# Performance work log

Measured on AMD Instinct MI355X. Metric: run time of the kernel, lower is better.

The kernel has to match this reference:

```python
import jax, jax.numpy as jnp
import numpy as np

B, T, F, H, OUT, L = 4096, 336, 12, 50, 1, 3


def _lstm_layer(x_tbf, W_ih, W_hh, b_ih, b_hh):
    """PyTorch-semantics LSTM layer. x_tbf: [T,B,in]; returns [T,B,H]."""
    Hh = W_hh.shape[1]
    Bsz = x_tbf.shape[1]
    # precompute input projection for all timesteps: [T,B,4H]
    xz = jnp.einsum('tbf,gf->tbg', x_tbf, W_ih) + (b_ih + b_hh)

    def step(carry, xz_t):
        h, c = carry
        z = xz_t + h @ W_hh.T  # [B,4H]
        i, f, g, o = jnp.split(z, 4, axis=-1)  # PyTorch gate order i,f,g,o
        c = jax.nn.sigmoid(f) * c + jax.nn.sigmoid(i) * jnp.tanh(g)
        h = jax.nn.sigmoid(o) * jnp.tanh(c)
        return (h, c), h

    h0 = jnp.zeros((Bsz, Hh), x_tbf.dtype)
    c0 = jnp.zeros((Bsz, Hh), x_tbf.dtype)
    _, hs = jax.lax.scan(step, (h0, c0), xz)
    return hs


def setup_inputs() -> dict:
    key = jax.random.key(0)
    ks = jax.random.split(key, 16)
    s = 1.0 / np.sqrt(H)  # PyTorch LSTM init scale
    inp = {"x": jax.random.normal(ks[0], (B, T, F), dtype=jnp.float32)}
    in_sizes = [F, H, H]
    k = 1
    for l in range(L):
        inp[f"W_ih_{l}"] = jax.random.uniform(ks[k], (4 * H, in_sizes[l]), jnp.float32, -s, s); k += 1
        inp[f"W_hh_{l}"] = jax.random.uniform(ks[k], (4 * H, H), jnp.float32, -s, s); k += 1
        inp[f"b_ih_{l}"] = jax.random.uniform(ks[k], (4 * H,), jnp.float32, -s, s); k += 1
        inp[f"b_hh_{l}"] = jax.random.uniform(ks[k], (4 * H,), jnp.float32, -s, s); k += 1
    inp["W_lin"] = jax.random.uniform(ks[13], (OUT, H), jnp.float32, -s, s)
    inp["b_lin"] = jax.random.uniform(ks[14], (OUT,), jnp.float32, -s, s)
    return inp


def reference(x, W_ih_0, W_hh_0, b_ih_0, b_hh_0,
              W_ih_1, W_hh_1, b_ih_1, b_hh_1,
              W_ih_2, W_hh_2, b_ih_2, b_hh_2,
              W_lin, b_lin):
    h = jnp.transpose(x, (1, 0, 2))  # [T,B,F] time-major for scan
    params = [(W_ih_0, W_hh_0, b_ih_0, b_hh_0),
              (W_ih_1, W_hh_1, b_ih_1, b_hh_1),
              (W_ih_2, W_hh_2, b_ih_2, b_hh_2)]
    for W_ih, W_hh, bi, bh in params:
        h = _lstm_layer(h, W_ih, W_hh, bi, bh)  # [T,B,H]
    last = h[-1]  # out[:, -1, :] in batch_first layout
    return last @ W_lin.T + b_lin  # [B,OUT]
```

## Files before the change

### kernel.cpp

```cpp
#include <hip/hip_runtime.h>


#define Bsz 4096
#define Tt  336
#define BT  16
#define NTH 1024
#define NTILE 13

typedef _Float16 half8 __attribute__((ext_vector_type(8)));
typedef float    floatx4 __attribute__((ext_vector_type(4)));

struct __align__(16) SMem {
  _Float16 act0[2][BT * 64];
  _Float16 act1[2][BT * 128];
  _Float16 act2[2][BT * 128];
};

__device__ __forceinline__ int offA0(int n, int L) {
  return n * 64 + ((((L >> 3) ^ n) & 7) << 3) + (L & 7);
}
__device__ __forceinline__ int offA12(int n, int L) {
  return n * 128 + ((((L >> 3) ^ n) & 15) << 3) + (L & 7);
}

__device__ __forceinline__ float lstm_cell(floatx4 z, float& c) {
  float ei = __builtin_amdgcn_exp2f(z[0]);
  float ef = __builtin_amdgcn_exp2f(z[1]);
  float eg = __builtin_amdgcn_exp2f(z[2]);
  float eo = __builtin_amdgcn_exp2f(z[3]);
  float ig = __builtin_amdgcn_rcpf(1.f + ei);
  float fg = __builtin_amdgcn_rcpf(1.f + ef);
  float rg = __builtin_amdgcn_rcpf(1.f + eg);
  float og = __builtin_amdgcn_rcpf(1.f + eo);
  float gg = 1.f - 2.f * rg;
  c = fg * c + ig * gg;
  float ec = __builtin_amdgcn_exp2f(2.885390082f * c);
  float rc = __builtin_amdgcn_rcpf(1.f + ec);
  return og * (1.f - 2.f * rc);
}

__device__ __forceinline__ half8 wfrag(const float* __restrict__ Wih,
                                       const float* __restrict__ Whh,
                                       int lenih, int bound, int R, int k0) {
  half8 r = {};
  int u = R >> 2, g = R & 3;
  float sc = (g == 2) ? 2.885390082f : -1.442695041f;
  if (u < 50) {
    int row = g * 50 + u;
#pragma unroll
    for (int j = 0; j < 8; ++j) {
      int k = k0 + j;
      float v = 0.f;
      if (k < bound)           v = Wih[row * lenih + k];
      else if (k < bound + 50) v = Whh[row * 50 + (k - bound)];
      r[j] = (_Float16)(sc * v);
    }
  }
  return r;
}

#define MFMA(a, b, acc) __builtin_amdgcn_mfma_f32_16x16x32_f16((a), (b), (acc), 0, 0, 0)

__global__ __launch_bounds__(NTH, 4)
void lstm_mfma_kernel(const float* __restrict__ x,
                      const float* __restrict__ Wih0, const float* __restrict__ Whh0,
                      const float* __restrict__ bih0, const float* __restrict__ bhh0,
                      const float* __restrict__ Wih1, const float* __restrict__ Whh1,
                      const float* __restrict__ bih1, const float* __restrict__ bhh1,
                      const float* __restrict__ Wih2, const float* __restrict__ Whh2,
                      const float* __restrict__ bih2, const float* __restrict__ bhh2,
                      const float* __restrict__ Wlin, const float* __restrict__ blin,
                      float* __restrict__ out) {
  __shared__ SMem sm;
  const int tid  = threadIdx.x;
  const int blk  = blockIdx.x;
  const int lane = tid & 63;
  const int w    = tid >> 6;
  const int n    = lane & 15;
  const int q    = lane >> 4;
  const bool hasTile = (w < NTILE);
  const int u    = 4 * w + q;
  const bool uok = hasTile && (u < 50);
  const int uc   = (u < 50) ? u : 0;

  {
    int* zp = (int*)&sm;
    for (int i = tid; i < (int)(sizeof(SMem) / 4); i += NTH) zp[i] = 0;
  }

  half8 a0f[2] = {}, a1f[4] = {}, a2f[4] = {};
  floatx4 bia0 = {0,0,0,0}, bia1 = {0,0,0,0}, bia2 = {0,0,0,0};
  if (hasTile) {
    int R = 16 * w + n;
#pragma unroll
    for (int kc = 0; kc < 2; ++kc)
      a0f[kc] = wfrag(Wih0, Whh0, 12, 12, R, kc * 32 + q * 8);
#pragma unroll
    for (int kc = 0; kc < 4; ++kc) {
      a1f[kc] = wfrag(Wih1, Whh1, 50, 50, R, kc * 32 + q * 8);
      a2f[kc] = wfrag(Wih2, Whh2, 50, 50, R, kc * 32 + q * 8);
    }
    if (u < 50) {
#pragma unroll
      for (int g = 0; g < 4; ++g) {
        float sc = (g == 2) ? 2.885390082f : -1.442695041f;
        bia0[g] = sc * (bih0[g * 50 + u] + bhh0[g * 50 + u]);
        bia1[g] = sc * (bih1[g * 50 + u] + bhh1[g * 50 + u]);
        bia2[g] = sc * (bih2[g * 50 + u] + bhh2[g * 50 + u]);
      }
    }
  }

  const int ro0[2] = { offA0(n, q * 8), offA0(n, 32 + q * 8) };
  const int ro1[4] = { offA12(n, q * 8),      offA12(n, 32 + q * 8),
                       offA12(n, 64 + q * 8), offA12(n, 96 + q * 8) };
  const int wr0 = offA0 (n, 12 + uc);
  const int wrA = offA12(n, uc);
  const int wrB = offA12(n, 50 + uc);

  const int tid0 = tid - NTILE * 64;
  const int sr = (tid0 >= 0) ? tid0 / 12 : 0;
  const int sf = (tid0 >= 0) ? tid0 - sr * 12 : 0;
  const int sxo = offA0(sr, sf);
  const float* xp = x + ((size_t)(blk * BT + sr) * Tt) * 12 + sf;
  float xnext = 0.f;

  __syncthreads();
  if (!hasTile) {
    sm.act0[0][sxo] = (_Float16)xp[0];
    xnext = xp[12];
  }
  __syncthreads();

  float c0 = 0.f, c1 = 0.f, c2 = 0.f;

#define STEP(p, t)                                                         \
  {                                                                        \
    if (hasTile) {                                                         \
      half8 b0 = *(const half8*)&sm.act0[p][ro0[0]];                       \
      half8 b1 = *(const half8*)&sm.act0[p][ro0[1]];                       \
      floatx4 z = bia0;                                                    \
      z = MFMA(a0f[0], b0, z);                                             \
      z = MFMA(a0f[1], b1, z);                                             \
      float h = lstm_cell(z, c0);                                          \
      _Float16 hh = (_Float16)h;                                           \
      if (uok) { sm.act0[1 - (p)][wr0] = hh; sm.act1[p][wrA] = hh; }       \
    } else {                                                               \
      if ((t) + 1 < Tt) sm.act0[1 - (p)][sxo] = (_Float16)xnext;           \
      xnext = ((t) + 2 < Tt) ? xp[((t) + 2) * 12] : 0.f;                   \
    }                                                                      \
    __syncthreads();                                                       \
    if (hasTile) {                                                         \
      half8 b0 = *(const half8*)&sm.act1[p][ro1[0]];                       \
      half8 b1 = *(const half8*)&sm.act1[p][ro1[1]];                       \
      half8 b2 = *(const half8*)&sm.act1[p][ro1[2]];                       \
      half8 b3 = *(const half8*)&sm.act1[p][ro1[3]];                       \
      floatx4 z = bia1;                                                    \
      z = MFMA(a1f[0], b0, z);                                             \
      z = MFMA(a1f[1], b1, z);                                             \
      z = MFMA(a1f[2], b2, z);                                             \
      z = MFMA(a1f[3], b3, z);                                             \
      float h = lstm_cell(z, c1);                                          \
      _Float16 hh = (_Float16)h;                                           \
      if (uok) { sm.act1[1 - (p)][wrB] = hh; sm.act2[p][wrA] = hh; }       \
    }                                                                      \
    __syncthreads();                                                       \
    if (hasTile) {                                                         \
      half8 b0 = *(const half8*)&sm.act2[p][ro1[0]];                       \
      half8 b1 = *(const half8*)&sm.act2[p][ro1[1]];                       \
      half8 b2 = *(const half8*)&sm.act2[p][ro1[2]];                       \
      half8 b3 = *(const half8*)&sm.act2[p][ro1[3]];                       \
      floatx4 z = bia2;                                                    \
      z = MFMA(a2f[0], b0, z);                                             \
      z = MFMA(a2f[1], b1, z);                                             \
      z = MFMA(a2f[2], b2, z);                                             \
      z = MFMA(a2f[3], b3, z);                                             \
      float h = lstm_cell(z, c2);                                          \
      if (uok) sm.act2[1 - (p)][wrB] = (_Float16)h;                        \
    }                                                                      \
     \
     \
     \
  }

  for (int t = 0; t < Tt; t += 2) {
    STEP(0, t)
    STEP(1, t + 1)
  }
#undef STEP

  __syncthreads();

  if (tid < BT) {
    float s = blin[0];
    for (int uu = 0; uu < 50; ++uu)
      s += Wlin[uu] * (float)sm.act2[0][offA12(tid, 50 + uu)];
    out[blk * BT + tid] = s;
  }
}

extern "C" void kernel_launch(void* const* d_in, const int* in_sizes, int n_in,
                              void* d_out, int out_size, void* d_ws, size_t ws_size,
                              hipStream_t stream) {
  const float* x    = (const float*)d_in[0];
  const float* Wih0 = (const float*)d_in[1];
  const float* Whh0 = (const float*)d_in[2];
  const float* bih0 = (const float*)d_in[3];
  const float* bhh0 = (const float*)d_in[4];
  const float* Wih1 = (const float*)d_in[5];
  const float* Whh1 = (const float*)d_in[6];
  const float* bih1 = (const float*)d_in[7];
  const float* bhh1 = (const float*)d_in[8];
  const float* Wih2 = (const float*)d_in[9];
  const float* Whh2 = (const float*)d_in[10];
  const float* bih2 = (const float*)d_in[11];
  const float* bhh2 = (const float*)d_in[12];
  const float* Wlin = (const float*)d_in[13];
  const float* blin = (const float*)d_in[14];
  float* outp = (float*)d_out;

  dim3 grid(Bsz / BT);
  dim3 block(NTH);
  lstm_mfma_kernel<<<grid, block, 0, stream>>>(
      x, Wih0, Whh0, bih0, bhh0, Wih1, Whh1, bih1, bhh1,
      Wih2, Whh2, bih2, bhh2, Wlin, blin, outp);
}
```

Baseline: 477.0 us.

## Wavefront-pipeline the three LSTM layers across timesteps with one barrier per tick

Replaces the per-timestep sequence of three layer stages separated by three barriers with a diagonal wavefront schedule. At each tick, layer 0 runs step t, layer 1 runs step t-1 and layer 2 runs step t-2. All three read their inputs from the previous tick's buffers, so only one __syncthreads is needed per tick and the MFMA chains of the three layers can overlap. A prologue and an epilogue fill and drain the pipeline, adding two extra ticks. Buffer parity for the inter-layer handoff changes to write the 1-p slot, which must line up exactly with the skewed indices.

```diff
diff --git a/kernel.cpp b/kernel.cpp
--- a/kernel.cpp
+++ b/kernel.cpp
@@ -134,62 +134,72 @@
 
   float c0 = 0.f, c1 = 0.f, c2 = 0.f;
 
-#define STEP(p, t)                                                         \
+#define TICK(p, DO0, DO1, DO2, t0)                                         \
   {                                                                        \
     if (hasTile) {                                                         \
-      half8 b0 = *(const half8*)&sm.act0[p][ro0[0]];                       \
-      half8 b1 = *(const half8*)&sm.act0[p][ro0[1]];                       \
-      floatx4 z = bia0;                                                    \
-      z = MFMA(a0f[0], b0, z);                                             \
-      z = MFMA(a0f[1], b1, z);                                             \
-      float h = lstm_cell(z, c0);                                          \
-      _Float16 hh = (_Float16)h;                                           \
-      if (uok) { sm.act0[1 - (p)][wr0] = hh; sm.act1[p][wrA] = hh; }       \
+      half8 b00{}, b01{}, b10{}, b11{}, b12{}, b13{};                      \
+      half8 b20{}, b21{}, b22{}, b23{};                                    \
+      if (DO0) {                                                           \
+        b00 = *(const half8*)&sm.act0[p][ro0[0]];                          \
+        b01 = *(const half8*)&sm.act0[p][ro0[1]];                          \
+      }                                                                    \
+      if (DO1) {                                                           \
+        b10 = *(const half8*)&sm.act1[p][ro1[0]];                          \
+        b11 = *(const half8*)&sm.act1[p][ro1[1]];                          \
+        b12 = *(const half8*)&sm.act1[p][ro1[2]];                          \
+        b13 = *(const half8*)&sm.act1[p][ro1[3]];                          \
+      }                                                                    \
+      if (DO2) {                                                           \
+        b20 = *(const half8*)&sm.act2[p][ro1[0]];                          \
+        b21 = *(const half8*)&sm.act2[p][ro1[1]];                          \
+        b22 = *(const half8*)&sm.act2[p][ro1[2]];                          \
+        b23 = *(const half8*)&sm.act2[p][ro1[3]];                          \
+      }                                                                    \
+      if (DO0) {                                                           \
+        floatx4 z = bia0;                                                  \
+        z = MFMA(a0f[0], b00, z);                                          \
+        z = MFMA(a0f[1], b01, z);                                          \
+        float h = lstm_cell(z, c0);                                        \
+        _Float16 hh = (_Float16)h;                                         \
+        if (uok) { sm.act0[1 - (p)][wr0] = hh;                             \
+                   sm.act1[1 - (p)][wrA] = hh; }                           \
+      }                                                                    \
+      if (DO1) {                                                           \
+        floatx4 z = bia1;                                                  \
+        z = MFMA(a1f[0], b10, z);                                          \
+        z = MFMA(a1f[1], b11, z);                                          \
+        z = MFMA(a1f[2], b12, z);                                          \
+        z = MFMA(a1f[3], b13, z);                                          \
+        float h = lstm_cell(z, c1);                                        \
+        _Float16 hh = (_Float16)h;                                         \
+        if (uok) { sm.act1[1 - (p)][wrB] = hh;                             \
+                   sm.act2[1 - (p)][wrA] = hh; }                           \
+      }                                                                    \
+      if (DO2) {                                                           \
+        floatx4 z = bia2;                                                  \
+        z = MFMA(a2f[0], b20, z);                                          \
+        z = MFMA(a2f[1], b21, z);                                          \
+        z = MFMA(a2f[2], b22, z);                                          \
+        z = MFMA(a2f[3], b23, z);                                          \
+        float h = lstm_cell(z, c2);                                        \
+        if (uok) sm.act2[1 - (p)][wrB] = (_Float16)h;                      \
+      }                                                                    \
     } else {                                                               \
-      if ((t) + 1 < Tt) sm.act0[1 - (p)][sxo] = (_Float16)xnext;           \
-      xnext = ((t) + 2 < Tt) ? xp[((t) + 2) * 12] : 0.f;                   \
+      if ((t0) + 1 < Tt) sm.act0[1 - (p)][sxo] = (_Float16)xnext;          \
+      xnext = ((t0) + 2 < Tt) ? xp[((t0) + 2) * 12] : 0.f;                 \
     }                                                                      \
     __syncthreads();                                                       \
-    if (hasTile) {                                                         \
-      half8 b0 = *(const half8*)&sm.act1[p][ro1[0]];                       \
-      half8 b1 = *(const half8*)&sm.act1[p][ro1[1]];                       \
-      half8 b2 = *(const half8*)&sm.act1[p][ro1[2]];                       \
-      half8 b3 = *(const half8*)&sm.act1[p][ro1[3]];                       \
-      floatx4 z = bia1;                                                    \
-      z = MFMA(a1f[0], b0, z);                                             \
-      z = MFMA(a1f[1], b1, z);                                             \
-      z = MFMA(a1f[2], b2, z);                                             \
-      z = MFMA(a1f[3], b3, z);                                             \
-      float h = lstm_cell(z, c1);                                          \
-      _Float16 hh = (_Float16)h;                                           \
-      if (uok) { sm.act1[1 - (p)][wrB] = hh; sm.act2[p][wrA] = hh; }       \
-    }                                                                      \
-    __syncthreads();                                                       \
-    if (hasTile) {                                                         \
-      half8 b0 = *(const half8*)&sm.act2[p][ro1[0]];                       \
-      half8 b1 = *(const half8*)&sm.act2[p][ro1[1]];                       \
-      half8 b2 = *(const half8*)&sm.act2[p][ro1[2]];                       \
-      half8 b3 = *(const half8*)&sm.act2[p][ro1[3]];                       \
-      floatx4 z = bia2;                                                    \
-      z = MFMA(a2f[0], b0, z);                                             \
-      z = MFMA(a2f[1], b1, z);                                             \
-      z = MFMA(a2f[2], b2, z);                                             \
-      z = MFMA(a2f[3], b3, z);                                             \
-      float h = lstm_cell(z, c2);                                          \
-      if (uok) sm.act2[1 - (p)][wrB] = (_Float16)h;                        \
-    }                                                                      \
-     \
-     \
-     \
-  }
-
-  for (int t = 0; t < Tt; t += 2) {
-    STEP(0, t)
-    STEP(1, t + 1)
-  }
-#undef STEP
-
-  __syncthreads();
+  }
+
+  TICK(0, 1, 0, 0, 0)
+  TICK(1, 1, 1, 0, 1)
+  for (int t = 2; t < Tt; t += 2) {
+    TICK(0, 1, 1, 1, t)
+    TICK(1, 1, 1, 1, t + 1)
+  }
+  TICK(0, 0, 1, 1, 336)
+  TICK(1, 0, 0, 1, 337)
+#undef TICK
 
   if (tid < BT) {
     float s = blin[0];
```

Result: faster. 459.5 us (-3.7%).

## Wavefront-pipeline the three LSTM layers across warps with one barrier per tick

Applied to the files above, without the earlier changes.

Before, 13 warps computed all three layers one after another inside each timestep, with two barriers between layers and three per step in total. Now the 16 warps are split by layer: each warp owns 2–3 gate tiles of a single layer. The layers run skewed in time, so layer l handles timestep t−l in the same tick, and each tick needs only one barrier. The input loading moves to threads 0–191, which also do tile work. The cost is extra prologue and epilogue ticks, more MFMA work per warp, divergent per-warp layer branches, and more registers per warp for up to 3 weight tiles.

```diff
diff --git a/kernel.cpp b/kernel.cpp
--- a/kernel.cpp
+++ b/kernel.cpp
@@ -5,7 +5,6 @@
 #define Tt  336
 #define BT  16
 #define NTH 1024
-#define NTILE 13
 
 typedef _Float16 half8 __attribute__((ext_vector_type(8)));
 typedef float    floatx4 __attribute__((ext_vector_type(4)));
@@ -78,35 +77,66 @@
   const int w    = tid >> 6;
   const int n    = lane & 15;
   const int q    = lane >> 4;
-  const bool hasTile = (w < NTILE);
-  const int u    = 4 * w + q;
-  const bool uok = hasTile && (u < 50);
-  const int uc   = (u < 50) ? u : 0;
 
   {
     int* zp = (int*)&sm;
     for (int i = tid; i < (int)(sizeof(SMem) / 4); i += NTH) zp[i] = 0;
   }
 
-  half8 a0f[2] = {}, a1f[4] = {}, a2f[4] = {};
-  floatx4 bia0 = {0,0,0,0}, bia1 = {0,0,0,0}, bia2 = {0,0,0,0};
-  if (hasTile) {
-    int R = 16 * w + n;
-#pragma unroll
-    for (int kc = 0; kc < 2; ++kc)
-      a0f[kc] = wfrag(Wih0, Whh0, 12, 12, R, kc * 32 + q * 8);
-#pragma unroll
-    for (int kc = 0; kc < 4; ++kc) {
-      a1f[kc] = wfrag(Wih1, Whh1, 50, 50, R, kc * 32 + q * 8);
-      a2f[kc] = wfrag(Wih2, Whh2, 50, 50, R, kc * 32 + q * 8);
-    }
-    if (u < 50) {
-#pragma unroll
-      for (int g = 0; g < 4; ++g) {
-        float sc = (g == 2) ? 2.885390082f : -1.442695041f;
-        bia0[g] = sc * (bih0[g * 50 + u] + bhh0[g * 50 + u]);
-        bia1[g] = sc * (bih1[g * 50 + u] + bhh1[g * 50 + u]);
-        bia2[g] = sc * (bih2[g * 50 + u] + bhh2[g * 50 + u]);
+  int Lw, nc, mm3[3] = {0, 0, 0};
+  switch (w) {
+    case 0:  Lw = 0; nc = 3; mm3[0] = 0;  mm3[1] = 1;  mm3[2] = 2;  break;
+    case 1:  Lw = 0; nc = 2; mm3[0] = 3;  mm3[1] = 4;               break;
+    case 2:  Lw = 0; nc = 3; mm3[0] = 5;  mm3[1] = 6;  mm3[2] = 7;  break;
+    case 3:  Lw = 0; nc = 2; mm3[0] = 8;  mm3[1] = 9;               break;
+    case 4:  Lw = 1; nc = 2; mm3[0] = 0;  mm3[1] = 1;               break;
+    case 5:  Lw = 1; nc = 3; mm3[0] = 2;  mm3[1] = 3;  mm3[2] = 4;  break;
+    case 6:  Lw = 1; nc = 2; mm3[0] = 5;  mm3[1] = 6;               break;
+    case 7:  Lw = 1; nc = 3; mm3[0] = 7;  mm3[1] = 8;  mm3[2] = 9;  break;
+    case 8:  Lw = 2; nc = 3; mm3[0] = 0;  mm3[1] = 1;  mm3[2] = 2;  break;
+    case 9:  Lw = 2; nc = 2; mm3[0] = 3;  mm3[1] = 4;               break;
+    case 10: Lw = 2; nc = 2; mm3[0] = 5;  mm3[1] = 6;               break;
+    case 11: Lw = 2; nc = 2; mm3[0] = 7;  mm3[1] = 8;               break;
+    case 12: Lw = 2; nc = 2; mm3[0] = 9;  mm3[1] = 10;              break;
+    case 13: Lw = 0; nc = 3; mm3[0] = 10; mm3[1] = 11; mm3[2] = 12; break;
+    case 14: Lw = 1; nc = 3; mm3[0] = 10; mm3[1] = 11; mm3[2] = 12; break;
+    default: Lw = 2; nc = 2; mm3[0] = 11; mm3[1] = 12;              break;
+  }
+  const float* Wih = (Lw == 0) ? Wih0 : ((Lw == 1) ? Wih1 : Wih2);
+  const float* Whh = (Lw == 0) ? Whh0 : ((Lw == 1) ? Whh1 : Whh2);
+  const float* bih = (Lw == 0) ? bih0 : ((Lw == 1) ? bih1 : bih2);
+  const float* bhh = (Lw == 0) ? bhh0 : ((Lw == 1) ? bhh1 : bhh2);
+  const int lenih = (Lw == 0) ? 12 : 50;
+  const int nkc   = (Lw == 0) ? 2 : 4;
+
+  half8  af[3][4];
+  floatx4 bia[3];
+  float  cst[3] = {0.f, 0.f, 0.f};
+  int    woA[3], woB[3];
+  bool   uokk[3];
+#pragma unroll
+  for (int i = 0; i < 3; ++i) {
+    bia[i] = (floatx4){0, 0, 0, 0};
+#pragma unroll
+    for (int kc = 0; kc < 4; ++kc) af[i][kc] = (half8){};
+    int m = mm3[i];
+    int u = 4 * m + q;
+    int uc = (u < 50) ? u : 49;
+    uokk[i] = (i < nc) && (u < 50);
+    if (Lw == 0) { woA[i] = offA0 (n, 12 + uc); woB[i] = offA12(n, uc); }
+    else         { woA[i] = offA12(n, 50 + uc); woB[i] = offA12(n, uc); }
+    if (i < nc) {
+      int R = 16 * m + n;
+#pragma unroll
+      for (int kc = 0; kc < 4; ++kc)
+        if (kc < nkc)
+          af[i][kc] = wfrag(Wih, Whh, lenih, lenih, R, kc * 32 + q * 8);
+      if (u < 50) {
+#pragma unroll
+        for (int g = 0; g < 4; ++g) {
+          float sc = (g == 2) ? 2.885390082f : -1.442695041f;
+          bia[i][g] = sc * (bih[g * 50 + u] + bhh[g * 50 + u]);
+        }
       }
     }
   }
@@ -114,82 +144,88 @@
   const int ro0[2] = { offA0(n, q * 8), offA0(n, 32 + q * 8) };
   const int ro1[4] = { offA12(n, q * 8),      offA12(n, 32 + q * 8),
                        offA12(n, 64 + q * 8), offA12(n, 96 + q * 8) };
-  const int wr0 = offA0 (n, 12 + uc);
-  const int wrA = offA12(n, uc);
-  const int wrB = offA12(n, 50 + uc);
-
-  const int tid0 = tid - NTILE * 64;
-  const int sr = (tid0 >= 0) ? tid0 / 12 : 0;
-  const int sf = (tid0 >= 0) ? tid0 - sr * 12 : 0;
+
+  const int sr = (tid < 192) ? tid / 12 : 0;
+  const int sf = (tid < 192) ? tid - sr * 12 : 0;
   const int sxo = offA0(sr, sf);
   const float* xp = x + ((size_t)(blk * BT + sr) * Tt) * 12 + sf;
   float xnext = 0.f;
 
   __syncthreads();
-  if (!hasTile) {
+  if (tid < 192) {
     sm.act0[0][sxo] = (_Float16)xp[0];
     xnext = xp[12];
   }
   __syncthreads();
 
-  float c0 = 0.f, c1 = 0.f, c2 = 0.f;
-
-#define STEP(p, t)                                                         \
+#define TICK(p, TAU, CHK)                                                  \
   {                                                                        \
-    if (hasTile) {                                                         \
-      half8 b0 = *(const half8*)&sm.act0[p][ro0[0]];                       \
-      half8 b1 = *(const half8*)&sm.act0[p][ro0[1]];                       \
-      floatx4 z = bia0;                                                    \
-      z = MFMA(a0f[0], b0, z);                                             \
-      z = MFMA(a0f[1], b1, z);                                             \
-      float h = lstm_cell(z, c0);                                          \
-      _Float16 hh = (_Float16)h;                                           \
-      if (uok) { sm.act0[1 - (p)][wr0] = hh; sm.act1[p][wrA] = hh; }       \
+    if (Lw == 0) {                                                         \
+      if (!(CHK) || (TAU) <= 335) {                                        \
+        half8 b0 = *(const half8*)&sm.act0[p][ro0[0]];                     \
+        half8 b1 = *(const half8*)&sm.act0[p][ro0[1]];                     \
+        for (int i = 0; i < 3; ++i) if (i < nc) {                          \
+          floatx4 z = bia[i];                                              \
+          z = MFMA(af[i][0], b0, z);                                       \
+          z = MFMA(af[i][1], b1, z);                                       \
+          float h = lstm_cell(z, cst[i]);                                  \
+          _Float16 hh = (_Float16)h;                                       \
+          if (uokk[i]) { sm.act0[1 - (p)][woA[i]] = hh;                    \
+                         sm.act1[1 - (p)][woB[i]] = hh; }                  \
+        }                                                                  \
+      }                                                                    \
+    } else if (Lw == 1) {                                                  \
+      if (!(CHK) || ((TAU) >= 1 && (TAU) <= 336)) {                        \
+        half8 b0 = *(const half8*)&sm.act1[p][ro1[0]];                     \
+        half8 b1 = *(const half8*)&sm.act1[p][ro1[1]];                     \
+        half8 b2 = *(const half8*)&sm.act1[p][ro1[2]];                     \
+        half8 b3 = *(const half8*)&sm.act1[p][ro1[3]];                     \
+        for (int i = 0; i < 3; ++i) if (i < nc) {                          \
+          floatx4 z = bia[i];                                              \
+          z = MFMA(af[i][0], b0, z);                                       \
+          z = MFMA(af[i][1], b1, z);                                       \
+          z = MFMA(af[i][2], b2, z);                                       \
+          z = MFMA(af[i][3], b3, z);                                       \
+          float h = lstm_cell(z, cst[i]);                                  \
+          _Float16 hh = (_Float16)h;                                       \
+          if (uokk[i]) { sm.act1[1 - (p)][woA[i]] = hh;                    \
+                         sm.act2[1 - (p)][woB[i]] = hh; }                  \
+        }                                                                  \
+      }                                                                    \
     } else {                                                               \
-      if ((t) + 1 < Tt) sm.act0[1 - (p)][sxo] = (_Float16)xnext;           \
-      xnext = ((t) + 2 < Tt) ? xp[((t) + 2) * 12] : 0.f;                   \
+      if (!(CHK) || ((TAU) >= 2)) {                                        \
+        half8 b0 = *(const half8*)&sm.act2[p][ro1[0]];                     \
+        half8 b1 = *(const half8*)&sm.act2[p][ro1[1]];                     \
+        half8 b2 = *(const half8*)&sm.act2[p][ro1[2]];                     \
+        half8 b3 = *(const half8*)&sm.act2[p][ro1[3]];                     \
+        for (int i = 0; i < 3; ++i) if (i < nc) {                          \
+          floatx4 z = bia[i];                                              \
+          z = MFMA(af[i][0], b0, z);                                       \
+          z = MFMA(af[i][1], b1, z);                                       \
+          z = MFMA(af[i][2], b2, z);                                       \
+          z = MFMA(af[i][3], b3, z);                                       \
+          float h = lstm_cell(z, cst[i]);                                  \
+          if (uokk[i]) sm.act2[1 - (p)][woA[i]] = (_Float16)h;             \
+        }                                                                  \
+      }                                                                    \
+    }                                                                      \
+    if (tid < 192) {                                                       \
+      if ((TAU) + 1 < Tt) sm.act0[1 - (p)][sxo] = (_Float16)xnext;         \
+      xnext = ((TAU) + 2 < Tt) ? xp[((TAU) + 2) * 12] : 0.f;               \
     }                                                                      \
     __syncthreads();                                                       \
-    if (hasTile) {                                                         \
-      half8 b0 = *(const half8*)&sm.act1[p][ro1[0]];                       \
-      half8 b1 = *(const half8*)&sm.act1[p][ro1[1]];                       \
-      half8 b2 = *(const half8*)&sm.act1[p][ro1[2]];                       \
-      half8 b3 = *(const half8*)&sm.act1[p][ro1[3]];                       \
-      floatx4 z = bia1;                                                    \
-      z = MFMA(a1f[0], b0, z);                                             \
-      z = MFMA(a1f[1], b1, z);                                             \
-      z = MFMA(a1f[2], b2, z);                                             \
-      z = MFMA(a1f[3], b3, z);                                             \
-      float h = lstm_cell(z, c1);                                          \
-      _Float16 hh = (_Float16)h;                                           \
-      if (uok) { sm.act1[1 - (p)][wrB] = hh; sm.act2[p][wrA] = hh; }       \
-    }                                                                      \
-    __syncthreads();                                                       \
-    if (hasTile) {                                                         \
-      half8 b0 = *(const half8*)&sm.act2[p][ro1[0]];                       \
-      half8 b1 = *(const half8*)&sm.act2[p][ro1[1]];                       \
-      half8 b2 = *(const half8*)&sm.act2[p][ro1[2]];                       \
-      half8 b3 = *(const half8*)&sm.act2[p][ro1[3]];                       \
-      floatx4 z = bia2;                                                    \
-      z = MFMA(a2f[0], b0, z);                                             \
-      z = MFMA(a2f[1], b1, z);                                             \
-      z = MFMA(a2f[2], b2, z);                                             \
-      z = MFMA(a2f[3], b3, z);                                             \
-      float h = lstm_cell(z, c2);                                          \
-      if (uok) sm.act2[1 - (p)][wrB] = (_Float16)h;                        \
-    }                                                                      \
-     \
-     \
-     \
-  }
-
-  for (int t = 0; t < Tt; t += 2) {
-    STEP(0, t)
-    STEP(1, t + 1)
-  }
-#undef STEP
-
-  __syncthreads();
+  }
+
+  TICK(0, 0, 1)
+  TICK(1, 1, 1)
+#pragma unroll 1
+  for (int t = 2; t < Tt; t += 2) {
+    TICK(0, t, 0)
+    TICK(1, t + 1, 0)
+  }
+  TICK(0, 336, 1)
+  TICK(1, 337, 1)
+#undef TICK
 
   if (tid < BT) {
     float s = blin[0];
```

After: 405.4 us. 15.0% less time.
